# Performance work log

Measured on AMD Instinct MI355X. Metric: run time of the kernel, lower is better.

## Reference

```python
import jax, jax.numpy as jnp
import numpy as np

IN_FEATURES = 4096
OUT_FEATURES = 4096
BATCH, SEQ = 8, 2048


def setup_inputs() -> dict:
    key = jax.random.key(0)
    k_in, k_w, k_b = jax.random.split(key, 3)
    inputs = {
        "input": jax.random.normal(k_in, (BATCH, SEQ, IN_FEATURES), dtype=jnp.float32),
        # int8-valued weights stored as int32 (range [-128, 127])
        "quantized_weight": jax.random.randint(k_w, (OUT_FEATURES, IN_FEATURES), -128, 128, dtype=jnp.int32),
        "weight_scale": jnp.array([0.01], dtype=jnp.float32),
        "weight_zero_point": jnp.array([2], dtype=jnp.int32),
        # int16-valued bias stored as int32 (range [-32768, 32767])
        "quantized_bias": jax.random.randint(k_b, (OUT_FEATURES,), -32768, 32768, dtype=jnp.int32),
        "bias_scale": jnp.array([0.0005], dtype=jnp.float32),
        "bias_zero_point": jnp.array([1], dtype=jnp.int32),
    }
    return inputs


def reference(input, quantized_weight, weight_scale, weight_zero_point,
              quantized_bias, bias_scale, bias_zero_point) -> jnp.ndarray:
    # Dequantize weights: (q - zp) * scale  -> [out, in] fp32
    w = (quantized_weight.astype(jnp.float32) - weight_zero_point.astype(jnp.float32)) * weight_scale
    # Dequantize bias -> [out] fp32
    b = (quantized_bias.astype(jnp.float32) - bias_zero_point.astype(jnp.float32)) * bias_scale
    # F.linear: input @ w.T + b ; input [B, S, in] -> out [B, S, out]
    return jnp.einsum('bsi,oi->bso', input, w) + b
```

## Files before the change

kernel.cpp:

```cpp
#include <hip/hip_runtime.h>

#define M_DIM 16384
#define N_DIM 4096
#define K_DIM 4096
#define BK 64
#define NKT (K_DIM / BK)

typedef unsigned char u8;
typedef __attribute__((ext_vector_type(4))) int   i32x4;

__global__ __launch_bounds__(256)
void quant_a_kernel(const float* __restrict__ in, char* __restrict__ out,
                    float* __restrict__ srow, int* __restrict__ rsum) {
    const int row  = blockIdx.x;
    const int t    = threadIdx.x;
    const int lane = t & 63, wv = t >> 6;
    const float4* rp = (const float4*)(in + (size_t)row * K_DIM);

    float4 v[4];
#pragma unroll
    for (int j = 0; j < 4; ++j) v[j] = rp[t * 4 + j];

    float amax = 0.f;
#pragma unroll
    for (int j = 0; j < 4; ++j) {
        amax = fmaxf(amax, fmaxf(fmaxf(fabsf(v[j].x), fabsf(v[j].y)),
                                 fmaxf(fabsf(v[j].z), fabsf(v[j].w))));
    }
#pragma unroll
    for (int off = 32; off; off >>= 1) amax = fmaxf(amax, __shfl_xor(amax, off));
    __shared__ float wred[4];
    __shared__ int   sred[4];
    if (lane == 0) wred[wv] = amax;
    __syncthreads();
    amax = fmaxf(fmaxf(wred[0], wred[1]), fmaxf(wred[2], wred[3]));
    const float inv = amax > 0.f ? 127.f / amax : 0.f;

    int lsum = 0;
    int pk[4];
#pragma unroll
    for (int j = 0; j < 4; ++j) {
        int q0 = __float2int_rn(v[j].x * inv);
        int q1 = __float2int_rn(v[j].y * inv);
        int q2 = __float2int_rn(v[j].z * inv);
        int q3 = __float2int_rn(v[j].w * inv);
        lsum += q0 + q1 + q2 + q3;
        pk[j] = (int)((unsigned)(q0 & 0xFF) | ((unsigned)(q1 & 0xFF) << 8) |
                      ((unsigned)(q2 & 0xFF) << 16) | ((unsigned)(q3 & 0xFF) << 24));
    }
    {
        const int mt = row >> 4, r = row & 15;
        const int kt = t >> 2,  j = t & 3;
        const size_t off = ((size_t)mt * NKT + kt) * 1024 + (size_t)(j * 16 + r) * 16;
        i32x4 w; w[0] = pk[0]; w[1] = pk[1]; w[2] = pk[2]; w[3] = pk[3];
        *(i32x4*)(out + off) = w;
    }
#pragma unroll
    for (int off = 32; off; off >>= 1) lsum += __shfl_xor(lsum, off);
    if (lane == 0) sred[wv] = lsum;
    __syncthreads();
    if (t == 0) {
        rsum[row] = sred[0] + sred[1] + sred[2] + sred[3];
        srow[row] = amax > 0.f ? amax / 127.f : 1.f;
    }
}

__global__ __launch_bounds__(256)
void pack_w_kernel(const int* __restrict__ q, char* __restrict__ out) {
    const int o = blockIdx.x;
    const int t = threadIdx.x;
    const int4* qp = (const int4*)(q + (size_t)o * K_DIM);
    int pk[4];
#pragma unroll
    for (int j = 0; j < 4; ++j) {
        int4 a = qp[t * 4 + j];
        pk[j] = (int)((unsigned)(a.x & 0xFF) | ((unsigned)(a.y & 0xFF) << 8) |
                      ((unsigned)(a.z & 0xFF) << 16) | ((unsigned)(a.w & 0xFF) << 24));
    }
    const int nt = o >> 4, r = o & 15;
    const int kt = t >> 2, j = t & 3;
    const size_t off = ((size_t)nt * NKT + kt) * 1024 + (size_t)(j * 16 + r) * 16;
    i32x4 w; w[0] = pk[0]; w[1] = pk[1]; w[2] = pk[2]; w[3] = pk[3];
    *(i32x4*)(out + off) = w;
}

__global__ __launch_bounds__(256, 2)
void gemm_i8_kernel(const char* __restrict__ Ap, const char* __restrict__ Wp,
                    const float* __restrict__ srow, const int* __restrict__ rsum,
                    const float* __restrict__ wsc_p, const int* __restrict__ wzp_p,
                    const int* __restrict__ qb, const float* __restrict__ bsc_p,
                    const int* __restrict__ bzp_p, float* __restrict__ C) {
    const int nwg = gridDim.x;
    const int cpx = nwg >> 3;
    const int bid = blockIdx.x;
    const int swz = (bid & 7) * cpx + (bid >> 3);
    const int st = swz >> 5, wi = swz & 31;
    const int bm = (st >> 2) * 8 + (wi >> 2);
    const int bn = (st & 3) * 4 + (wi & 3);
    const int m0 = bm * 128, n0 = bn * 256;

    const int tid  = threadIdx.x;
    const int wv   = tid >> 6;
    const int lane = tid & 63;
    const int l15  = lane & 15;

    const char* Aft = Ap + ((size_t)(bm * 8) * NKT) * 1024 + lane * 16;
    const char* Wft = Wp + ((size_t)(bn * 16 + wv * 4) * NKT) * 1024 + lane * 16;

    i32x4 acc[8][4] = {};

    for (int u = 0; u < NKT; ++u) {
        i32x4 af[8], bfr[4];
#pragma unroll
        for (int mi = 0; mi < 8; ++mi)
            af[mi] = *(const i32x4*)(Aft + ((size_t)mi * NKT + u) * 1024);
#pragma unroll
        for (int ni = 0; ni < 4; ++ni)
            bfr[ni] = *(const i32x4*)(Wft + ((size_t)ni * NKT + u) * 1024);

        __builtin_amdgcn_s_setprio(1);
#pragma unroll
        for (int mi = 0; mi < 8; ++mi)
#pragma unroll
            for (int ni = 0; ni < 4; ++ni)
                acc[mi][ni] = __builtin_amdgcn_mfma_i32_16x16x64_i8(
                    af[mi], bfr[ni], acc[mi][ni], 0, 0, 0);
        __builtin_amdgcn_s_setprio(0);
    }

    const float ws  = wsc_p[0];
    const float zpf = (float)wzp_p[0];
    const float bsc = bsc_p[0];
    const float bzp = (float)bzp_p[0];
    float bias_[4];
#pragma unroll
    for (int ni = 0; ni < 4; ++ni) {
        int col = n0 + wv * 64 + ni * 16 + l15;
        bias_[ni] = ((float)qb[col] - bzp) * bsc;
    }
#pragma unroll
    for (int mi = 0; mi < 8; ++mi) {
        int rbase = m0 + mi * 16 + (lane >> 4) * 4;
        float fs_[4], fc_[4];
#pragma unroll
        for (int i = 0; i < 4; ++i) {
            float sf = ws * srow[rbase + i];
            fs_[i] = sf;
            fc_[i] = -sf * zpf * (float)rsum[rbase + i];
        }
#pragma unroll
        for (int ni = 0; ni < 4; ++ni) {
            int col = n0 + wv * 64 + ni * 16 + l15;
#pragma unroll
            for (int i = 0; i < 4; ++i)
                C[(size_t)(rbase + i) * N_DIM + col] =
                    fs_[i] * (float)acc[mi][ni][i] + fc_[i] + bias_[ni];
        }
    }
}

__global__ void gemm_fallback_kernel(const float* __restrict__ A, const int* __restrict__ Wq,
                                     const float* __restrict__ wsc_p, const int* __restrict__ wzp_p,
                                     const int* __restrict__ qb, const float* __restrict__ bsc_p,
                                     const int* __restrict__ bzp_p, float* __restrict__ C) {
    int m = blockIdx.y;
    int n = blockIdx.x * 256 + threadIdx.x;
    float zp = (float)wzp_p[0];
    float sc = wsc_p[0];
    __shared__ float Arow[512];
    float acc = 0.f;
    for (int k0 = 0; k0 < K_DIM; k0 += 512) {
        __syncthreads();
        for (int t = threadIdx.x; t < 512; t += 256)
            Arow[t] = A[(size_t)m * K_DIM + k0 + t];
        __syncthreads();
        const int4* wp = (const int4*)(Wq + (size_t)n * K_DIM + k0);
        for (int kk = 0; kk < 512; kk += 4) {
            int4 q = wp[kk >> 2];
            acc += Arow[kk]     * ((float)q.x - zp);
            acc += Arow[kk + 1] * ((float)q.y - zp);
            acc += Arow[kk + 2] * ((float)q.z - zp);
            acc += Arow[kk + 3] * ((float)q.w - zp);
        }
    }
    acc *= sc;
    acc += ((float)qb[n] - (float)bzp_p[0]) * bsc_p[0];
    C[(size_t)m * N_DIM + n] = acc;
}

extern "C" void kernel_launch(void* const* d_in, const int* in_sizes, int n_in,
                              void* d_out, int out_size, void* d_ws, size_t ws_size,
                              hipStream_t stream) {
    (void)in_sizes; (void)n_in; (void)out_size;
    const float* input = (const float*)d_in[0];
    const int*   qw    = (const int*)d_in[1];
    const float* wsc   = (const float*)d_in[2];
    const int*   wzp   = (const int*)d_in[3];
    const int*   qb    = (const int*)d_in[4];
    const float* bsc   = (const float*)d_in[5];
    const int*   bzp   = (const int*)d_in[6];
    float* out = (float*)d_out;

    size_t offA = 0;
    size_t offW = (size_t)M_DIM * K_DIM;
    size_t offS = offW + (size_t)N_DIM * K_DIM;
    size_t offR = offS + (size_t)M_DIM * sizeof(float);
    size_t need = offR + (size_t)M_DIM * sizeof(int);

    if (ws_size >= need) {
        char*  Aq = (char*)d_ws + offA;
        char*  Wq8 = (char*)d_ws + offW;
        float* S  = (float*)((char*)d_ws + offS);
        int*   R  = (int*)((char*)d_ws + offR);
        quant_a_kernel<<<M_DIM, 256, 0, stream>>>(input, Aq, S, R);
        pack_w_kernel<<<N_DIM, 256, 0, stream>>>(qw, Wq8);
        gemm_i8_kernel<<<(M_DIM / 128) * (N_DIM / 256), 256, 0, stream>>>(
            Aq, Wq8, S, R, wsc, wzp, qb, bsc, bzp, out);
    } else {
        dim3 grid(N_DIM / 256, M_DIM);
        gemm_fallback_kernel<<<grid, 256, 0, stream>>>(input, qw, wsc, wzp, qb, bsc, bzp, out);
    }
}
```

Baseline: 413.5 us.

## Stage A tiles through LDS with async global_load_lds multi-buffer pipeline

The quantization kernel now writes A as plain row-major int8 with coalesced loads, replacing the pre-tiled fragment layout. The GEMM shares each A tile across the four waves through a 4-slot LDS ring filled by global_load_lds, prefetched three iterations ahead and guarded by vmcnt waits and barriers. Before, every wave loaded the same A fragments straight from global memory. This cuts redundant global traffic for A but adds barriers and depends on the vmcnt counting being right, since W loads share the same counter.

```diff
diff --git a/kernel.cpp b/kernel.cpp
--- a/kernel.cpp
+++ b/kernel.cpp
@@ -8,6 +8,9 @@
 
 typedef unsigned char u8;
 typedef __attribute__((ext_vector_type(4))) int   i32x4;
+
+#define AS1 __attribute__((address_space(1)))
+#define AS3 __attribute__((address_space(3)))
 
 __global__ __launch_bounds__(256)
 void quant_a_kernel(const float* __restrict__ in, char* __restrict__ out,
@@ -19,7 +22,7 @@
 
     float4 v[4];
 #pragma unroll
-    for (int j = 0; j < 4; ++j) v[j] = rp[t * 4 + j];
+    for (int j = 0; j < 4; ++j) v[j] = rp[t + 256 * j];
 
     float amax = 0.f;
 #pragma unroll
@@ -37,7 +40,7 @@
     const float inv = amax > 0.f ? 127.f / amax : 0.f;
 
     int lsum = 0;
-    int pk[4];
+    unsigned* orow = (unsigned*)(out + (size_t)row * K_DIM);
 #pragma unroll
     for (int j = 0; j < 4; ++j) {
         int q0 = __float2int_rn(v[j].x * inv);
@@ -45,15 +48,9 @@
         int q2 = __float2int_rn(v[j].z * inv);
         int q3 = __float2int_rn(v[j].w * inv);
         lsum += q0 + q1 + q2 + q3;
-        pk[j] = (int)((unsigned)(q0 & 0xFF) | ((unsigned)(q1 & 0xFF) << 8) |
-                      ((unsigned)(q2 & 0xFF) << 16) | ((unsigned)(q3 & 0xFF) << 24));
-    }
-    {
-        const int mt = row >> 4, r = row & 15;
-        const int kt = t >> 2,  j = t & 3;
-        const size_t off = ((size_t)mt * NKT + kt) * 1024 + (size_t)(j * 16 + r) * 16;
-        i32x4 w; w[0] = pk[0]; w[1] = pk[1]; w[2] = pk[2]; w[3] = pk[3];
-        *(i32x4*)(out + off) = w;
+        unsigned pk = (unsigned)(q0 & 0xFF) | ((unsigned)(q1 & 0xFF) << 8) |
+                      ((unsigned)(q2 & 0xFF) << 16) | ((unsigned)(q3 & 0xFF) << 24);
+        orow[t + 256 * j] = pk;
     }
 #pragma unroll
     for (int off = 32; off; off >>= 1) lsum += __shfl_xor(lsum, off);
@@ -85,11 +82,13 @@
 }
 
 __global__ __launch_bounds__(256, 2)
-void gemm_i8_kernel(const char* __restrict__ Ap, const char* __restrict__ Wp,
+void gemm_i8_kernel(const char* __restrict__ Aq, const char* __restrict__ Wp,
                     const float* __restrict__ srow, const int* __restrict__ rsum,
                     const float* __restrict__ wsc_p, const int* __restrict__ wzp_p,
                     const int* __restrict__ qb, const float* __restrict__ bsc_p,
                     const int* __restrict__ bzp_p, float* __restrict__ C) {
+    __shared__ __align__(16) u8 ldsA[4 * 8192];
+
     const int nwg = gridDim.x;
     const int cpx = nwg >> 3;
     const int bid = blockIdx.x;
@@ -104,19 +103,39 @@
     const int lane = tid & 63;
     const int l15  = lane & 15;
 
-    const char* Aft = Ap + ((size_t)(bm * 8) * NKT) * 1024 + lane * 16;
+    const char* AgT = Aq + (size_t)(m0 + wv * 32 + l15) * K_DIM + ((lane >> 4) << 4);
     const char* Wft = Wp + ((size_t)(bn * 16 + wv * 4) * NKT) * 1024 + lane * 16;
 
     i32x4 acc[8][4] = {};
 
+    auto STAGE_A = [&](int ns, int u) {
+#pragma unroll
+        for (int i = 0; i < 2; ++i)
+            __builtin_amdgcn_global_load_lds(
+                (const AS1 void*)(AgT + (size_t)i * 16 * K_DIM + u * BK),
+                (AS3 void*)(ldsA + ns * 8192 + (wv * 2 + i) * 1024), 16, 0, 0);
+    };
+
+    STAGE_A(0, 0);
+    STAGE_A(1, 1);
+    STAGE_A(2, 2);
+    asm volatile("s_waitcnt vmcnt(4)" ::: "memory");
+    __builtin_amdgcn_s_barrier();
+
     for (int u = 0; u < NKT; ++u) {
-        i32x4 af[8], bfr[4];
-#pragma unroll
-        for (int mi = 0; mi < 8; ++mi)
-            af[mi] = *(const i32x4*)(Aft + ((size_t)mi * NKT + u) * 1024);
+        const u8* Asl = ldsA + (u & 3) * 8192;
+
+        i32x4 bfr[4];
 #pragma unroll
         for (int ni = 0; ni < 4; ++ni)
             bfr[ni] = *(const i32x4*)(Wft + ((size_t)ni * NKT + u) * 1024);
+
+        if (u + 3 < NKT) STAGE_A((u + 3) & 3, u + 3);
+
+        i32x4 af[8];
+#pragma unroll
+        for (int mi = 0; mi < 8; ++mi)
+            af[mi] = *(const i32x4*)(Asl + mi * 1024 + lane * 16);
 
         __builtin_amdgcn_s_setprio(1);
 #pragma unroll
@@ -126,6 +145,9 @@
                 acc[mi][ni] = __builtin_amdgcn_mfma_i32_16x16x64_i8(
                     af[mi], bfr[ni], acc[mi][ni], 0, 0, 0);
         __builtin_amdgcn_s_setprio(0);
+
+        asm volatile("s_waitcnt vmcnt(2)" ::: "memory");
+        __builtin_amdgcn_s_barrier();
     }
 
     const float ws  = wsc_p[0];
```

Result: faster. 390.4 us (-5.6%).
